# Kernel optimization log

Hardware: AMD Instinct MI355X
Metric: run time of the kernel (lower is better)

The kernel has to match this reference:

```python
import jax, jax.numpy as jnp
import numpy as np

BLOCK = 128
LN_EPS = 1e-5


def _dequant_linear(x, w, s):
    # w: [out, in], s: [out//128, in//128] block scales -> y = x @ (w * expand(s)).T
    ws = w * jnp.repeat(jnp.repeat(s, BLOCK, axis=0), BLOCK, axis=1)
    return x @ ws.T


def setup_inputs() -> dict:
    H, L, M, S, N = 2048, 8192, 4096, 1024, 8192
    key = jax.random.key(0)
    ks = jax.random.split(key, 12)
    sc = 0.02  # weight init scale to keep activations sane
    return {
        "x": jax.random.normal(ks[0], (N, H), dtype=jnp.float32),
        "w_qkv": jax.random.normal(ks[1], (L, H), dtype=jnp.float32) * sc,
        "s_qkv": jnp.ones((L // BLOCK, H // BLOCK), dtype=jnp.float32),
        "w_z": jax.random.normal(ks[2], (M, H), dtype=jnp.float32) * sc,
        "s_z": jnp.ones((M // BLOCK, H // BLOCK), dtype=jnp.float32),
        "w_b": jax.random.normal(ks[3], (S, H), dtype=jnp.float32) * sc,
        "s_b": jnp.ones((S // BLOCK, H // BLOCK), dtype=jnp.float32),
        "w_a": jax.random.normal(ks[4], (S, H), dtype=jnp.float32) * sc,
        "s_a": jnp.ones((S // BLOCK, H // BLOCK), dtype=jnp.float32),
        "d_qkv": jax.random.normal(ks[5], (H, L), dtype=jnp.float32) * sc,
        "d_z": jax.random.normal(ks[6], (H, M), dtype=jnp.float32) * sc,
        "d_b": jax.random.normal(ks[7], (H, S), dtype=jnp.float32) * sc,
        "d_a": jax.random.normal(ks[8], (H, S), dtype=jnp.float32) * sc,
        "gamma": jnp.ones((H,), dtype=jnp.float32),
        "beta": jnp.zeros((H,), dtype=jnp.float32),
    }


def reference(x, w_qkv, s_qkv, w_z, s_z, w_b, s_b, w_a, s_a,
              d_qkv, d_z, d_b, d_a, gamma, beta):
    qkv = _dequant_linear(x, w_qkv, s_qkv) @ d_qkv.T
    z = _dequant_linear(x, w_z, s_z) @ d_z.T
    b = _dequant_linear(x, w_b, s_b) @ d_b.T
    a = _dequant_linear(x, w_a, s_a) @ d_a.T
    h = qkv + z + b + a
    mu = jnp.mean(h, axis=-1, keepdims=True)
    var = jnp.mean(jnp.square(h - mu), axis=-1, keepdims=True)
    return (h - mu) * jax.lax.rsqrt(var + LN_EPS) * gamma + beta
```

## Files before the change

### kernel.cpp

```cpp
#include <hip/hip_runtime.h>
#include <hip/hip_bf16.h>
#include <stdint.h>


typedef unsigned short u16;
typedef __bf16 bf16x8 __attribute__((ext_vector_type(8)));
typedef float f32x4 __attribute__((ext_vector_type(4)));

#define H 2048
#define KTOT 14336

__device__ __forceinline__ u16 f2b(float f) {
    union { float f; uint32_t u; } v; v.f = f;
    uint32_t u = v.u;
    return (u16)((u + 0x7fffu + ((u >> 16) & 1u)) >> 16);
}

__device__ __forceinline__ void gld16(const u16* g, u16* l) {
    __builtin_amdgcn_global_load_lds((__attribute__((address_space(1))) void*)g,
                                     (__attribute__((address_space(3))) void*)l,
                                     16, 0, 0);
}

__global__ __launch_bounds__(256) void prep_pack(const float* __restrict__ dq,
                                                 const float* __restrict__ dz,
                                                 const float* __restrict__ db,
                                                 const float* __restrict__ da,
                                                 const float* __restrict__ x,
                                                 u16* __restrict__ Acat,
                                                 u16* __restrict__ Xb) {
    int bid = blockIdx.x;
    if (bid >= 28672) {
        size_t i = (((size_t)(bid - 28672)) * 256 + threadIdx.x) * 8;
        float4 a = *(const float4*)(x + i);
        float4 b = *(const float4*)(x + i + 4);
        uint32_t p0 = (uint32_t)f2b(a.x) | ((uint32_t)f2b(a.y) << 16);
        uint32_t p1 = (uint32_t)f2b(a.z) | ((uint32_t)f2b(a.w) << 16);
        uint32_t p2 = (uint32_t)f2b(b.x) | ((uint32_t)f2b(b.y) << 16);
        uint32_t p3 = (uint32_t)f2b(b.z) | ((uint32_t)f2b(b.w) << 16);
        *(uint4*)(Xb + i) = make_uint4(p0, p1, p2, p3);
        return;
    }
    const float* src; int kshift, kmask, coloff, base;
    if (bid < 16384)      { src = dq; kshift = 13; kmask = 8191; coloff = 0;     base = 0; }
    else if (bid < 24576) { src = dz; kshift = 12; kmask = 4095; coloff = 8192;  base = 16384; }
    else if (bid < 26624) { src = db; kshift = 10; kmask = 1023; coloff = 12288; base = 24576; }
    else                  { src = da; kshift = 10; kmask = 1023; coloff = 13312; base = 26624; }
    size_t idx = ((size_t)(bid - base) * 256 + threadIdx.x) * 4;
    int r = (int)(idx >> kshift);
    int c = (int)(idx & (size_t)kmask);
    float4 v = *(const float4*)(src + idx);
    ushort4 o = make_ushort4(f2b(v.x), f2b(v.y), f2b(v.z), f2b(v.w));
    *(ushort4*)(Acat + (size_t)r * KTOT + coloff + c) = o;
}

__global__ __launch_bounds__(256) void prep_w(const float* __restrict__ wq, const float* __restrict__ sq,
                                              const float* __restrict__ wz, const float* __restrict__ sz,
                                              const float* __restrict__ wb, const float* __restrict__ sb,
                                              const float* __restrict__ wa, const float* __restrict__ sa,
                                              u16* __restrict__ dst) {
    __shared__ float tile[64][65];
    int by = blockIdx.y;
    const float* w; const float* s; int coloff, ybase;
    if (by < 128)      { w = wq; s = sq; coloff = 0;     ybase = 0; }
    else if (by < 192) { w = wz; s = sz; coloff = 8192;  ybase = 128; }
    else if (by < 208) { w = wb; s = sb; coloff = 12288; ybase = 192; }
    else               { w = wa; s = sa; coloff = 13312; ybase = 208; }
    const int t = threadIdx.x;
    const int i0 = blockIdx.x * 64, k0 = (by - ybase) * 64;
    const int c4 = (t & 15) * 4;
    const int r0 = t >> 4;
    const int sib = i0 >> 7;
#pragma unroll
    for (int rr = 0; rr < 4; ++rr) {
        int r = r0 + rr * 16;
        float sc = s[((k0 + r) >> 7) * (H / 128) + sib];
        float4 v = *(const float4*)(w + (size_t)(k0 + r) * H + i0 + c4);
        tile[r][c4 + 0] = v.x * sc;
        tile[r][c4 + 1] = v.y * sc;
        tile[r][c4 + 2] = v.z * sc;
        tile[r][c4 + 3] = v.w * sc;
    }
    __syncthreads();
#pragma unroll
    for (int rr = 0; rr < 4; ++rr) {
        int i = r0 + rr * 16;
        ushort4 o = make_ushort4(f2b(tile[c4 + 0][i]), f2b(tile[c4 + 1][i]),
                                 f2b(tile[c4 + 2][i]), f2b(tile[c4 + 3][i]));
        *(ushort4*)(dst + (size_t)(i0 + i) * KTOT + coloff + k0 + c4) = o;
    }
}

__global__ __launch_bounds__(256) void reduce4_cvt(const float* __restrict__ P,
                                                   u16* __restrict__ G) {
    size_t i = ((size_t)blockIdx.x * 256 + threadIdx.x) * 4;
    const size_t st = (size_t)H * H;
    float4 a = *(const float4*)(P + i);
    float4 b = *(const float4*)(P + i + st);
    float4 c = *(const float4*)(P + i + 2 * st);
    float4 d = *(const float4*)(P + i + 3 * st);
    ushort4 o = make_ushort4(f2b(a.x + b.x + c.x + d.x),
                             f2b(a.y + b.y + c.y + d.y),
                             f2b(a.z + b.z + c.z + d.z),
                             f2b(a.w + b.w + c.w + d.w));
    *(ushort4*)(G + i) = o;
}

__device__ __forceinline__ void gemm_core(const u16* __restrict__ A,
                                          const u16* __restrict__ B,
                                          float* __restrict__ C,
                                          int lda, int ldb, int N, int klen) {
    __shared__ __align__(16) u16 As[128 * 64];
    __shared__ __align__(16) u16 Bs[128 * 64];
    const int t = threadIdx.x;
    const int lane = t & 63;
    const int wave = t >> 6;
    const int wm = (wave >> 1) * 64;
    const int wn = (wave & 1) * 64;
    const size_t bm0 = (size_t)blockIdx.y * 128;
    const size_t bn0 = (size_t)blockIdx.x * 128;
    const int kstart = blockIdx.z * klen;

    const int srow = t >> 3;
    const int skc = (t & 7) ^ (srow & 7);
    const u16* ga = A + (bm0 + srow) * (size_t)lda + kstart + skc * 8;
    const u16* gb = B + (bn0 + srow) * (size_t)ldb + kstart + skc * 8;
    u16* la = As + (t & ~63) * 8;
    u16* lb = Bs + (t & ~63) * 8;
    const size_t lda32 = (size_t)32 * lda;
    const size_t ldb32 = (size_t)32 * ldb;

    f32x4 acc[4][4] = {};
    const int lr = lane & 15;
    const int c0 = ((lane >> 4) ^ (lane & 7)) * 8;
    const int c1 = ((4 + (lane >> 4)) ^ (lane & 7)) * 8;
    const u16* arow = As + (wm + lr) * 64;
    const u16* brow = Bs + (wn + lr) * 64;

    for (int kk = 0; kk < klen; kk += 64) {
        gld16(ga,              la);
        gld16(ga + lda32,      la + 2048);
        gld16(ga + 2 * lda32,  la + 4096);
        gld16(ga + 3 * lda32,  la + 6144);
        gld16(gb,              lb);
        gld16(gb + ldb32,      lb + 2048);
        gld16(gb + 2 * ldb32,  lb + 4096);
        gld16(gb + 3 * ldb32,  lb + 6144);
        ga += 64; gb += 64;
        __syncthreads();
        bf16x8 af[4], bfr[4];
#pragma unroll
        for (int i = 0; i < 4; ++i) {
            af[i]  = *(const bf16x8*)(arow + i * 1024 + c0);
            bfr[i] = *(const bf16x8*)(brow + i * 1024 + c0);
        }
#pragma unroll
        for (int mi = 0; mi < 4; ++mi)
#pragma unroll
            for (int ni = 0; ni < 4; ++ni)
                acc[mi][ni] = __builtin_amdgcn_mfma_f32_16x16x32_bf16(af[mi], bfr[ni], acc[mi][ni], 0, 0, 0);
#pragma unroll
        for (int i = 0; i < 4; ++i) {
            af[i]  = *(const bf16x8*)(arow + i * 1024 + c1);
            bfr[i] = *(const bf16x8*)(brow + i * 1024 + c1);
        }
#pragma unroll
        for (int mi = 0; mi < 4; ++mi)
#pragma unroll
            for (int ni = 0; ni < 4; ++ni)
                acc[mi][ni] = __builtin_amdgcn_mfma_f32_16x16x32_bf16(af[mi], bfr[ni], acc[mi][ni], 0, 0, 0);
        __syncthreads();
    }

    const int en = (int)bn0 + wn + (lane & 15);
    const int em = (int)bm0 + wm + (lane >> 4) * 4;
#pragma unroll
    for (int mi = 0; mi < 4; ++mi)
#pragma unroll
        for (int ni = 0; ni < 4; ++ni)
#pragma unroll
            for (int r = 0; r < 4; ++r)
                C[(size_t)(em + mi * 16 + r) * N + (en + ni * 16)] = acc[mi][ni][r];
}

__global__ __launch_bounds__(256, 4) void gemm_kb_part(const u16* __restrict__ A,
                                                       const u16* __restrict__ B,
                                                       float* __restrict__ C,
                                                       int lda, int ldb, int N, int klen) {
    gemm_core(A, B, C + (size_t)blockIdx.z * H * H, lda, ldb, N, klen);
}

__global__ __launch_bounds__(256, 4) void gemm_kc_store(const u16* __restrict__ A,
                                                        const u16* __restrict__ B,
                                                        float* __restrict__ C,
                                                        int lda, int ldb, int N, int klen) {
    gemm_core(A, B, C, lda, ldb, N, klen);
}

__global__ __launch_bounds__(256) void layernorm_kernel(float* __restrict__ h,
                                                        const float* __restrict__ gamma,
                                                        const float* __restrict__ beta) {
    const int t = threadIdx.x;
    float* row = h + (size_t)blockIdx.x * H;
    float4 v0 = ((const float4*)row)[t];
    float4 v1 = ((const float4*)row)[t + 256];
    float s = v0.x + v0.y + v0.z + v0.w + v1.x + v1.y + v1.z + v1.w;
    float q = v0.x * v0.x + v0.y * v0.y + v0.z * v0.z + v0.w * v0.w +
              v1.x * v1.x + v1.y * v1.y + v1.z * v1.z + v1.w * v1.w;
#pragma unroll
    for (int off = 32; off > 0; off >>= 1) {
        s += __shfl_down(s, off, 64);
        q += __shfl_down(q, off, 64);
    }
    __shared__ float sw[4], sq[4];
    if ((t & 63) == 0) { sw[t >> 6] = s; sq[t >> 6] = q; }
    __syncthreads();
    s = sw[0] + sw[1] + sw[2] + sw[3];
    q = sq[0] + sq[1] + sq[2] + sq[3];
    float mu = s * (1.0f / H);
    float var = q * (1.0f / H) - mu * mu;
    float rs = rsqrtf(var + 1e-5f);
    float4 g0 = ((const float4*)gamma)[t], g1 = ((const float4*)gamma)[t + 256];
    float4 b0 = ((const float4*)beta)[t],  b1 = ((const float4*)beta)[t + 256];
    v0.x = (v0.x - mu) * rs * g0.x + b0.x;
    v0.y = (v0.y - mu) * rs * g0.y + b0.y;
    v0.z = (v0.z - mu) * rs * g0.z + b0.z;
    v0.w = (v0.w - mu) * rs * g0.w + b0.w;
    v1.x = (v1.x - mu) * rs * g1.x + b1.x;
    v1.y = (v1.y - mu) * rs * g1.y + b1.y;
    v1.z = (v1.z - mu) * rs * g1.z + b1.z;
    v1.w = (v1.w - mu) * rs * g1.w + b1.w;
    ((float4*)row)[t] = v0;
    ((float4*)row)[t + 256] = v1;
}

extern "C" void kernel_launch(void* const* d_in, const int* in_sizes, int n_in,
                              void* d_out, int out_size, void* d_ws, size_t ws_size,
                              hipStream_t stream) {
    const float* x     = (const float*)d_in[0];
    const float* w_qkv = (const float*)d_in[1];
    const float* s_qkv = (const float*)d_in[2];
    const float* w_z   = (const float*)d_in[3];
    const float* s_z   = (const float*)d_in[4];
    const float* w_b   = (const float*)d_in[5];
    const float* s_b   = (const float*)d_in[6];
    const float* w_a   = (const float*)d_in[7];
    const float* s_a   = (const float*)d_in[8];
    const float* dq    = (const float*)d_in[9];
    const float* dz    = (const float*)d_in[10];
    const float* db    = (const float*)d_in[11];
    const float* da    = (const float*)d_in[12];
    const float* gamma = (const float*)d_in[13];
    const float* beta  = (const float*)d_in[14];
    float* out = (float*)d_out;

    uint8_t* ws = (uint8_t*)d_ws;
    u16* Acat = (u16*)(ws);
    u16* Bcat = (u16*)(ws + 58720256);
    u16* Xb   = (u16*)(ws + 117440512);
    u16* G    = (u16*)(ws + 150994944);

    prep_pack<<<36864, 256, 0, stream>>>(dq, dz, db, da, x, Acat, Xb);
    prep_w<<<dim3(32, 224), 256, 0, stream>>>(w_qkv, s_qkv, w_z, s_z,
                                              w_b, s_b, w_a, s_a, Bcat);
    gemm_kb_part<<<dim3(16, 16, 4), 256, 0, stream>>>(Acat, Bcat, out, KTOT, KTOT, H, 3584);
    reduce4_cvt<<<4096, 256, 0, stream>>>(out, G);
    gemm_kc_store<<<dim3(16, 64, 1), 256, 0, stream>>>(Xb, G, out, H, H, H, H);
    layernorm_kernel<<<8192, 256, 0, stream>>>(out, gamma, beta);
}
```

Baseline: 559.3 us.

## Use 256x256 GEMM tiles with 4-stage LDS prefetch pipeline and 512 threads

Replaces the 128x128 single-buffered GEMM core with a 256x256 tile per 512-thread block. The block uses four LDS stages of BK=32, prefetches three stages ahead and synchronises with explicit vmcnt waits, and raises wave priority around the MFMA bursts. This is meant to increase operand reuse per LDS load and hide global-to-LDS latency behind compute. The cost is 128 KB of LDS and large accumulator register use, which limits occupancy. The first GEMM's grid also drops to 256 blocks, which may leave compute units underused.

```diff
diff --git a/kernel.cpp b/kernel.cpp
--- a/kernel.cpp
+++ b/kernel.cpp
@@ -106,76 +106,90 @@
     *(ushort4*)(G + i) = o;
 }
 
-__device__ __forceinline__ void gemm_core(const u16* __restrict__ A,
-                                          const u16* __restrict__ B,
-                                          float* __restrict__ C,
-                                          int lda, int ldb, int N, int klen) {
-    __shared__ __align__(16) u16 As[128 * 64];
-    __shared__ __align__(16) u16 Bs[128 * 64];
+__device__ __forceinline__ void gemm256_core(const u16* __restrict__ A,
+                                             const u16* __restrict__ B,
+                                             float* __restrict__ C,
+                                             int lda, int ldb, int N, int klen) {
+    __shared__ __align__(16) u16 As[32768];
+    __shared__ __align__(16) u16 Bs[32768];
     const int t = threadIdx.x;
     const int lane = t & 63;
     const int wave = t >> 6;
-    const int wm = (wave >> 1) * 64;
-    const int wn = (wave & 1) * 64;
-    const size_t bm0 = (size_t)blockIdx.y * 128;
-    const size_t bn0 = (size_t)blockIdx.x * 128;
+    const int wm = (wave >> 2) * 128;
+    const int wn = (wave & 3) * 64;
+    const size_t bm0 = (size_t)blockIdx.y * 256;
+    const size_t bn0 = (size_t)blockIdx.x * 256;
     const int kstart = blockIdx.z * klen;
-
-    const int srow = t >> 3;
-    const int skc = (t & 7) ^ (srow & 7);
-    const u16* ga = A + (bm0 + srow) * (size_t)lda + kstart + skc * 8;
-    const u16* gb = B + (bn0 + srow) * (size_t)ldb + kstart + skc * 8;
-    u16* la = As + (t & ~63) * 8;
-    u16* lb = Bs + (t & ~63) * 8;
-    const size_t lda32 = (size_t)32 * lda;
-    const size_t ldb32 = (size_t)32 * ldb;
-
-    f32x4 acc[4][4] = {};
+    const int NS = klen >> 5;
+
+    const int srow = t >> 2;
+    const int scol = ((t & 3) ^ ((t >> 3) & 3)) * 8;
+    const u16* ga = A + (bm0 + srow) * (size_t)lda + kstart + scol;
+    const u16* gb = B + (bn0 + srow) * (size_t)ldb + kstart + scol;
+    const size_t lda128 = (size_t)128 * lda;
+    const size_t ldb128 = (size_t)128 * ldb;
+    u16* const lwa = As + (t & ~63) * 8;
+    u16* const lwb = Bs + (t & ~63) * 8;
+
     const int lr = lane & 15;
-    const int c0 = ((lane >> 4) ^ (lane & 7)) * 8;
-    const int c1 = ((4 + (lane >> 4)) ^ (lane & 7)) * 8;
-    const u16* arow = As + (wm + lr) * 64;
-    const u16* brow = Bs + (wn + lr) * 64;
-
-    for (int kk = 0; kk < klen; kk += 64) {
-        gld16(ga,              la);
-        gld16(ga + lda32,      la + 2048);
-        gld16(ga + 2 * lda32,  la + 4096);
-        gld16(ga + 3 * lda32,  la + 6144);
-        gld16(gb,              lb);
-        gld16(gb + ldb32,      lb + 2048);
-        gld16(gb + 2 * ldb32,  lb + 4096);
-        gld16(gb + 3 * ldb32,  lb + 6144);
-        ga += 64; gb += 64;
-        __syncthreads();
-        bf16x8 af[4], bfr[4];
-#pragma unroll
-        for (int i = 0; i < 4; ++i) {
-            af[i]  = *(const bf16x8*)(arow + i * 1024 + c0);
-            bfr[i] = *(const bf16x8*)(brow + i * 1024 + c0);
-        }
-#pragma unroll
-        for (int mi = 0; mi < 4; ++mi)
+    const int fro = (((lane >> 4) ^ ((lr >> 1) & 3))) * 8;
+    const u16* const fra = As + (wm + lr) * 32 + fro;
+    const u16* const frb = Bs + (wn + lr) * 32 + fro;
+
+    f32x4 acc[8][4] = {};
+
+    auto STAGE = [&](int sidx) {
+        const int sl = (sidx & 3) * 8192;
+        const u16* a = ga + (size_t)sidx * 32;
+        const u16* b = gb + (size_t)sidx * 32;
+        gld16(a,          lwa + sl);
+        gld16(a + lda128, lwa + sl + 4096);
+        gld16(b,          lwb + sl);
+        gld16(b + ldb128, lwb + sl + 4096);
+    };
+    auto COMPUTE = [&](int sidx) {
+        const int sl = (sidx & 3) * 8192;
+        const u16* fa = fra + sl;
+        const u16* fb = frb + sl;
+        bf16x8 af[8], bfr[4];
+#pragma unroll
+        for (int i = 0; i < 8; ++i) af[i] = *(const bf16x8*)(fa + i * 512);
+#pragma unroll
+        for (int j = 0; j < 4; ++j) bfr[j] = *(const bf16x8*)(fb + j * 512);
+        __builtin_amdgcn_s_setprio(1);
+#pragma unroll
+        for (int mi = 0; mi < 8; ++mi)
 #pragma unroll
             for (int ni = 0; ni < 4; ++ni)
                 acc[mi][ni] = __builtin_amdgcn_mfma_f32_16x16x32_bf16(af[mi], bfr[ni], acc[mi][ni], 0, 0, 0);
-#pragma unroll
-        for (int i = 0; i < 4; ++i) {
-            af[i]  = *(const bf16x8*)(arow + i * 1024 + c1);
-            bfr[i] = *(const bf16x8*)(brow + i * 1024 + c1);
-        }
-#pragma unroll
-        for (int mi = 0; mi < 4; ++mi)
-#pragma unroll
-            for (int ni = 0; ni < 4; ++ni)
-                acc[mi][ni] = __builtin_amdgcn_mfma_f32_16x16x32_bf16(af[mi], bfr[ni], acc[mi][ni], 0, 0, 0);
-        __syncthreads();
-    }
-
-    const int en = (int)bn0 + wn + (lane & 15);
+        __builtin_amdgcn_s_setprio(0);
+    };
+
+    STAGE(0); STAGE(1); STAGE(2);
+    int s = 0;
+    for (; s < NS - 3; ++s) {
+        STAGE(s + 3);
+        asm volatile("s_waitcnt vmcnt(12)" ::: "memory");
+        __builtin_amdgcn_s_barrier();
+        COMPUTE(s);
+        __builtin_amdgcn_s_barrier();
+    }
+    asm volatile("s_waitcnt vmcnt(8)" ::: "memory");
+    __builtin_amdgcn_s_barrier();
+    COMPUTE(s); ++s;
+    __builtin_amdgcn_s_barrier();
+    asm volatile("s_waitcnt vmcnt(4)" ::: "memory");
+    __builtin_amdgcn_s_barrier();
+    COMPUTE(s); ++s;
+    __builtin_amdgcn_s_barrier();
+    asm volatile("s_waitcnt vmcnt(0)" ::: "memory");
+    __builtin_amdgcn_s_barrier();
+    COMPUTE(s);
+
+    const int en = (int)bn0 + wn + lr;
     const int em = (int)bm0 + wm + (lane >> 4) * 4;
 #pragma unroll
-    for (int mi = 0; mi < 4; ++mi)
+    for (int mi = 0; mi < 8; ++mi)
 #pragma unroll
         for (int ni = 0; ni < 4; ++ni)
 #pragma unroll
@@ -183,18 +197,18 @@
                 C[(size_t)(em + mi * 16 + r) * N + (en + ni * 16)] = acc[mi][ni][r];
 }
 
-__global__ __launch_bounds__(256, 4) void gemm_kb_part(const u16* __restrict__ A,
+__global__ __launch_bounds__(512, 2) void gemm_kb_part(const u16* __restrict__ A,
                                                        const u16* __restrict__ B,
                                                        float* __restrict__ C,
                                                        int lda, int ldb, int N, int klen) {
-    gemm_core(A, B, C + (size_t)blockIdx.z * H * H, lda, ldb, N, klen);
-}
-
-__global__ __launch_bounds__(256, 4) void gemm_kc_store(const u16* __restrict__ A,
+    gemm256_core(A, B, C + (size_t)blockIdx.z * H * H, lda, ldb, N, klen);
+}
+
+__global__ __launch_bounds__(512, 2) void gemm_kc_store(const u16* __restrict__ A,
                                                         const u16* __restrict__ B,
                                                         float* __restrict__ C,
                                                         int lda, int ldb, int N, int klen) {
-    gemm_core(A, B, C, lda, ldb, N, klen);
+    gemm256_core(A, B, C, lda, ldb, N, klen);
 }
 
 __global__ __launch_bounds__(256) void layernorm_kernel(float* __restrict__ h,
@@ -263,8 +277,8 @@
     prep_pack<<<36864, 256, 0, stream>>>(dq, dz, db, da, x, Acat, Xb);
     prep_w<<<dim3(32, 224), 256, 0, stream>>>(w_qkv, s_qkv, w_z, s_z,
                                               w_b, s_b, w_a, s_a, Bcat);
-    gemm_kb_part<<<dim3(16, 16, 4), 256, 0, stream>>>(Acat, Bcat, out, KTOT, KTOT, H, 3584);
+    gemm_kb_part<<<dim3(8, 8, 4), 512, 0, stream>>>(Acat, Bcat, out, KTOT, KTOT, H, 3584);
     reduce4_cvt<<<4096, 256, 0, stream>>>(out, G);
-    gemm_kc_store<<<dim3(16, 64, 1), 256, 0, stream>>>(Xb, G, out, H, H, H, H);
+    gemm_kc_store<<<dim3(8, 32, 1), 512, 0, stream>>>(Xb, G, out, H, H, H, H);
     layernorm_kernel<<<8192, 256, 0, stream>>>(out, gamma, beta);
 }
```

After: 589.2 us. 5.3% more time.
